# Performance work log

Measured on AMD Instinct MI355X. Metric: run time of the kernel, lower is better.

The kernel has to match this reference:

```python
import jax, jax.numpy as jnp
import numpy as np

N = 50000      # nodes
E = 1_600_000  # edges (avg degree 32)
IN = 256
HID = 64
H = 4          # heads
OUT = 128
NEG = 0.2      # LeakyReLU negative slope


def setup_inputs() -> dict:
    key = jax.random.key(0)
    ks = jax.random.split(key, 16)
    def p(i, shape):
        return jax.random.normal(ks[i], shape, jnp.float32) * 0.05
    x = jax.random.normal(ks[0], (N, IN), jnp.float32)
    edge_index = jax.random.randint(ks[1], (2, E), 0, N, dtype=jnp.int64)
    return dict(
        x=x, edge_index=edge_index,
        W0=p(2, (IN, H * HID)), as0=p(3, (H, HID)), ad0=p(4, (H, HID)), b0=p(5, (H * HID,)),
        W1=p(6, (H * HID, H * HID)), as1=p(7, (H, HID)), ad1=p(8, (H, HID)), b1=p(9, (H * HID,)),
        W2=p(10, (H * HID, OUT)), as2=p(11, (1, OUT)), ad2=p(12, (1, OUT)), b2=p(13, (OUT,)),
        Wl=p(14, (H * HID, OUT)), bl=p(15, (OUT,)),
    )


def gat_conv(x, src, dst, W, a_s, a_d, b, heads, ch):
    # Linear projection -> per-head features [N, H, C]
    h = (x @ W).reshape(-1, heads, ch)
    # Per-node attention logits [N, H]
    al_s = jnp.einsum('nhc,hc->nh', h, a_s)
    al_d = jnp.einsum('nhc,hc->nh', h, a_d)
    # Per-edge logits: gather + LeakyReLU  [E2, H]
    e = jax.nn.leaky_relu(al_s[src] + al_d[dst], NEG)
    # Segment softmax over destination neighborhoods (stable)
    m = jax.ops.segment_max(e, dst, num_segments=N)
    e = jnp.exp(e - m[dst])
    s = jax.ops.segment_sum(e, dst, num_segments=N)
    a = e / s[dst]
    # Weighted scatter-add aggregation [N, H, C]
    out = jax.ops.segment_sum(a[:, :, None] * h[src], dst, num_segments=N)
    return out.reshape(N, heads * ch) + b


def reference(x, edge_index, W0, as0, ad0, b0, W1, as1, ad1, b1, W2, as2, ad2, b2, Wl, bl):
    # add self-loops (PyG GATConv default)
    loop = jnp.arange(N, dtype=edge_index.dtype)
    src = jnp.concatenate([edge_index[0], loop])
    dst = jnp.concatenate([edge_index[1], loop])
    # layer 0: in -> hid*heads (no residual at layer 0)
    h0 = gat_conv(x, src, dst, W0, as0, ad0, b0, H, HID)
    # layer 1: hid*heads -> hid*heads, residual
    h1 = gat_conv(h0, src, dst, W1, as1, ad1, b1, H, HID) + h0
    # layer 2 (last): hid*heads -> out with 1 head, residual via last_linear
    h2 = gat_conv(h1, src, dst, W2, as2, ad2, b2, 1, OUT) + (h1 @ Wl + bl)
    return h2
```

## Files before the change

kernel.cpp:

```cpp
#include <hip/hip_runtime.h>
#include <hip/hip_bf16.h>

#define N_NODES 50000
#define N_EDGES 1600000
#define E2 (N_EDGES + N_NODES)

typedef __attribute__((ext_vector_type(8))) short bf16x8;
typedef __attribute__((ext_vector_type(4))) float f32x4;

static __device__ __forceinline__ float lrelu(float x) { return x > 0.f ? x : 0.2f * x; }

static __device__ __forceinline__ float b2f(ushort u) {
    union { unsigned int u; float f; } v;
    v.u = ((unsigned int)u) << 16;
    return v.f;
}
static __device__ __forceinline__ float hi2f(unsigned int u) {
    union { unsigned int u; float f; } v;
    v.u = u & 0xffff0000u;
    return v.f;
}
static __device__ __forceinline__ float lo2f(unsigned int u) {
    union { unsigned int u; float f; } v;
    v.u = u << 16;
    return v.f;
}
static __device__ __forceinline__ ushort f2b(float f) {
    union { float f; unsigned int u; } v;
    v.f = f;
    unsigned int r = v.u + 0x7FFFu + ((v.u >> 16) & 1u);
    return (ushort)(r >> 16);
}


__global__ void k_deg(const int* __restrict__ edst, int* __restrict__ deg) {
    int e = blockIdx.x * blockDim.x + threadIdx.x;
    if (e >= E2) return;
    int d = (e < N_EDGES) ? edst[e] : (e - N_EDGES);
    atomicAdd(&deg[d], 1);
}

__global__ void k_scan1(const int* __restrict__ deg, int* __restrict__ rowptr, int* __restrict__ bsum) {
    __shared__ int sd[256];
    int t = threadIdx.x;
    int i = blockIdx.x * 256 + t;
    int v = (i < N_NODES) ? deg[i] : 0;
    sd[t] = v;
    __syncthreads();
    for (int off = 1; off < 256; off <<= 1) {
        int add = (t >= off) ? sd[t - off] : 0;
        __syncthreads();
        sd[t] += add;
        __syncthreads();
    }
    if (i < N_NODES) rowptr[i + 1] = sd[t];
    if (t == 255) bsum[blockIdx.x] = sd[255];
}

__global__ void k_scan2(const int* __restrict__ bsum, int* __restrict__ boff, int nb) {
    __shared__ int sd[256];
    int t = threadIdx.x;
    sd[t] = (t < nb) ? bsum[t] : 0;
    __syncthreads();
    for (int off = 1; off < 256; off <<= 1) {
        int add = (t >= off) ? sd[t - off] : 0;
        __syncthreads();
        sd[t] += add;
        __syncthreads();
    }
    if (t < nb) boff[t] = (t > 0) ? sd[t - 1] : 0;
}

__global__ void k_scan3(int* __restrict__ rowptr, int* __restrict__ cursor, const int* __restrict__ boff) {
    int i = blockIdx.x * 256 + threadIdx.x;
    if (i < N_NODES) {
        int r = rowptr[i + 1] + boff[blockIdx.x];
        rowptr[i + 1] = r;
        cursor[i + 1] = r;
    }
    if (i == 0) { rowptr[0] = 0; cursor[0] = 0; }
}

__global__ void k_fill(const int* __restrict__ esrc, const int* __restrict__ edst,
                       int* __restrict__ cursor, int* __restrict__ col) {
    int e = blockIdx.x * blockDim.x + threadIdx.x;
    if (e >= E2) return;
    int s, d;
    if (e < N_EDGES) { s = esrc[e]; d = edst[e]; } else { s = d = e - N_EDGES; }
    int pos = atomicAdd(&cursor[d], 1);
    col[pos] = s;
}


__global__ void k_quant(const float* __restrict__ x, ushort* __restrict__ xb, int n4) {
    int i = blockIdx.x * 256 + threadIdx.x;
    if (i >= n4) return;
    float4 v = ((const float4*)x)[i];
    ushort4 o;
    o.x = f2b(v.x); o.y = f2b(v.y); o.z = f2b(v.z); o.w = f2b(v.w);
    ((ushort4*)xb)[i] = o;
}

__global__ void k_wt(const float* __restrict__ W, ushort* __restrict__ Wt) {
    int i = blockIdx.x * 256 + threadIdx.x;
    int k = i >> 8, n = i & 255;
    Wt[n * 256 + k] = f2b(W[i]);
}

__global__ void k_wtc(const float* __restrict__ W2, const float* __restrict__ Wl, ushort* __restrict__ Wt) {
    int i = blockIdx.x * 256 + threadIdx.x;
    int k = i >> 8, n = i & 255;
    float v = (n < 128) ? W2[k * 128 + n] : Wl[k * 128 + (n - 128)];
    Wt[n * 256 + k] = f2b(v);
}


template <bool FUSE>
__global__ __launch_bounds__(256) void k_mfma(const ushort* __restrict__ A, const ushort* __restrict__ Bt,
                                              ushort* __restrict__ Cb, int M,
                                              const float* __restrict__ a_s, const float* __restrict__ a_d,
                                              float* __restrict__ als, float* __restrict__ ald) {
    const int t = threadIdx.x;
    const int w = t >> 6, l = t & 63;
    const int lr = l & 15, lk = l >> 4;
    const int m0 = blockIdx.x * 32;
    const int n0 = w * 64;
    f32x4 acc[2][4] = {};

    int r0 = m0 + lr;      if (r0 >= M) r0 = M - 1;
    int r1 = m0 + 16 + lr; if (r1 >= M) r1 = M - 1;
    const ushort* a0p = A + (size_t)r0 * 256 + lk * 8;
    const ushort* a1p = A + (size_t)r1 * 256 + lk * 8;
    const ushort* bp  = Bt + (size_t)(n0 + lr) * 256 + lk * 8;

#pragma unroll
    for (int k0 = 0; k0 < 256; k0 += 32) {
        bf16x8 a0 = *(const bf16x8*)(a0p + k0);
        bf16x8 a1 = *(const bf16x8*)(a1p + k0);
#pragma unroll
        for (int n = 0; n < 4; ++n) {
            bf16x8 b = *(const bf16x8*)(bp + n * 16 * 256 + k0);
            acc[0][n] = __builtin_amdgcn_mfma_f32_16x16x32_bf16(a0, b, acc[0][n], 0, 0, 0);
            acc[1][n] = __builtin_amdgcn_mfma_f32_16x16x32_bf16(a1, b, acc[1][n], 0, 0, 0);
        }
    }

#pragma unroll
    for (int m = 0; m < 2; ++m) {
#pragma unroll
        for (int r = 0; r < 4; ++r) {
            int row = m0 + m * 16 + lk * 4 + r;
            if (row >= M) continue;
#pragma unroll
            for (int n = 0; n < 4; ++n) {
                Cb[(size_t)row * 256 + n0 + n * 16 + lr] = f2b(acc[m][n][r]);
            }
        }
    }

    if constexpr (FUSE) {
        float asc[4], adc[4];
#pragma unroll
        for (int n = 0; n < 4; ++n) {
            int c = n0 + n * 16 + lr;
            asc[n] = a_s[c];
            adc[n] = a_d[c];
        }
#pragma unroll
        for (int m = 0; m < 2; ++m) {
#pragma unroll
            for (int r = 0; r < 4; ++r) {
                float pa = 0.f, pd = 0.f;
#pragma unroll
                for (int n = 0; n < 4; ++n) {
                    pa += acc[m][n][r] * asc[n];
                    pd += acc[m][n][r] * adc[n];
                }
#pragma unroll
                for (int off = 1; off < 16; off <<= 1) {
                    pa += __shfl_xor(pa, off);
                    pd += __shfl_xor(pd, off);
                }
                if (lr == 0) {
                    int row = m0 + m * 16 + lk * 4 + r;
                    if (row < M) {
                        als[row * 4 + w] = pa;
                        ald[row * 4 + w] = pd;
                    }
                }
            }
        }
    }
}


template <int HEADS, int CHAN>
__global__ __launch_bounds__(256) void k_al(const ushort* __restrict__ Pb,
                                            const float* __restrict__ a_s, const float* __restrict__ a_d,
                                            float* __restrict__ als, float* __restrict__ ald) {
    int n = blockIdx.x * 4 + (threadIdx.x >> 6);
    if (n >= N_NODES) return;
    int l = threadIdx.x & 63;
    const ushort* row = Pb + (size_t)n * 256;
#pragma unroll
    for (int h = 0; h < HEADS; ++h) {
        float ps = 0.f, pd = 0.f;
#pragma unroll
        for (int c = l; c < CHAN; c += 64) {
            float v = b2f(row[h * CHAN + c]);
            ps += v * a_s[h * CHAN + c];
            pd += v * a_d[h * CHAN + c];
        }
#pragma unroll
        for (int off = 32; off > 0; off >>= 1) {
            ps += __shfl_xor(ps, off);
            pd += __shfl_xor(pd, off);
        }
        if (l == 0) { als[n * HEADS + h] = ps; ald[n * HEADS + h] = pd; }
    }
}


template <int HEADS>
__device__ __forceinline__ void load_als(const float* __restrict__ als, int src, float* v) {
    if constexpr (HEADS == 4) {
        float4 a = *(const float4*)(als + (size_t)src * 4);
        v[0] = a.x; v[1] = a.y; v[2] = a.z; v[3] = a.w;
    } else {
        v[0] = als[src];
    }
}


template <int HEADS, int CHAN, bool RESB, bool LIN, bool WRITEF, bool WRITEB>
__global__ __launch_bounds__(256) void k_aggw(
    const ushort* __restrict__ Pb,
    const float* __restrict__ als, const float* __restrict__ ald,
    const int* __restrict__ rowptr, const int* __restrict__ col,
    const float* __restrict__ bias, const float* __restrict__ bias2,
    const ushort* __restrict__ residb, float* __restrict__ out, ushort* __restrict__ outb) {
    constexpr int BLK = HEADS * CHAN;
    constexpr int CPL = BLK / 64;
    const int t = threadIdx.x;
    const int w = t >> 6, l = t & 63;
    const int n = blockIdx.x * 4 + w;
    const int rs = rowptr[n];
    const int deg = rowptr[n + 1] - rs;

    __shared__ int s_src[4][64];
    __shared__ float s_w[4][64 * HEADS];

    float aldn[HEADS];
    load_als<HEADS>(ald, n, aldn);

    float acc[CPL];
#pragma unroll
    for (int c = 0; c < CPL; ++c) acc[c] = 0.f;
    float sw[HEADS];
#pragma unroll
    for (int h = 0; h < HEADS; ++h) sw[h] = 0.f;

    const int hsel = l >> 4;

    for (int base = 0; base < deg; base += 64) {
        int j = base + l;
        if (j < deg) {
            int src = col[rs + j];
            s_src[w][l] = src;
            float av[HEADS];
            load_als<HEADS>(als, src, av);
#pragma unroll
            for (int h = 0; h < HEADS; ++h) {
                float wv = __expf(lrelu(av[h] + aldn[h]));
                s_w[w][l * HEADS + h] = wv;
                sw[h] += wv;
            }
        }
        int cnt = min(64, deg - base);
        int jj = 0;
        for (; jj + 2 <= cnt; jj += 2) {
            int s0 = __builtin_amdgcn_readfirstlane(s_src[w][jj]);
            int s1 = __builtin_amdgcn_readfirstlane(s_src[w][jj + 1]);
            if constexpr (CPL == 4) {
                float w0 = s_w[w][jj * HEADS + hsel];
                float w1 = s_w[w][(jj + 1) * HEADS + hsel];
                uint2 v0 = *(const uint2*)(Pb + (size_t)s0 * 256 + l * 4);
                uint2 v1 = *(const uint2*)(Pb + (size_t)s1 * 256 + l * 4);
                acc[0] += w0 * lo2f(v0.x); acc[1] += w0 * hi2f(v0.x);
                acc[2] += w0 * lo2f(v0.y); acc[3] += w0 * hi2f(v0.y);
                acc[0] += w1 * lo2f(v1.x); acc[1] += w1 * hi2f(v1.x);
                acc[2] += w1 * lo2f(v1.y); acc[3] += w1 * hi2f(v1.y);
            } else {
                float w0 = s_w[w][jj];
                float w1 = s_w[w][jj + 1];
                unsigned int v0 = *(const unsigned int*)(Pb + (size_t)s0 * 256 + l * 2);
                unsigned int v1 = *(const unsigned int*)(Pb + (size_t)s1 * 256 + l * 2);
                acc[0] += w0 * lo2f(v0); acc[1] += w0 * hi2f(v0);
                acc[0] += w1 * lo2f(v1); acc[1] += w1 * hi2f(v1);
            }
        }
        if (jj < cnt) {
            int s0 = __builtin_amdgcn_readfirstlane(s_src[w][jj]);
            if constexpr (CPL == 4) {
                float w0 = s_w[w][jj * HEADS + hsel];
                uint2 v0 = *(const uint2*)(Pb + (size_t)s0 * 256 + l * 4);
                acc[0] += w0 * lo2f(v0.x); acc[1] += w0 * hi2f(v0.x);
                acc[2] += w0 * lo2f(v0.y); acc[3] += w0 * hi2f(v0.y);
            } else {
                float w0 = s_w[w][jj];
                unsigned int v0 = *(const unsigned int*)(Pb + (size_t)s0 * 256 + l * 2);
                acc[0] += w0 * lo2f(v0); acc[1] += w0 * hi2f(v0);
            }
        }
    }

#pragma unroll
    for (int off = 32; off > 0; off >>= 1)
#pragma unroll
        for (int h = 0; h < HEADS; ++h) sw[h] += __shfl_xor(sw[h], off);

    float stot;
    if constexpr (HEADS == 4) {
        stot = (hsel == 0) ? sw[0] : (hsel == 1) ? sw[1] : (hsel == 2) ? sw[2] : sw[3];
    } else {
        stot = sw[0];
    }
    float rinv = 1.0f / stot;

    float r[CPL];
#pragma unroll
    for (int c = 0; c < CPL; ++c) r[c] = acc[c] * rinv + bias[l * CPL + c];
    if constexpr (RESB) {
        ushort4 rv = *(const ushort4*)(residb + (size_t)n * 256 + l * 4);
        r[0] += b2f(rv.x); r[1] += b2f(rv.y); r[2] += b2f(rv.z); r[3] += b2f(rv.w);
    }
    if constexpr (LIN) {
        unsigned int lv = *(const unsigned int*)(Pb + (size_t)n * 256 + 128 + l * 2);
        float2 bv = *(const float2*)(bias2 + l * 2);
        r[0] += lo2f(lv) + bv.x;
        r[1] += hi2f(lv) + bv.y;
    }
    if constexpr (WRITEF) {
        if constexpr (CPL == 4) {
            *(float4*)&out[(size_t)n * BLK + l * 4] = make_float4(r[0], r[1], r[2], r[3]);
        } else {
            *(float2*)&out[(size_t)n * BLK + l * 2] = make_float2(r[0], r[1]);
        }
    }
    if constexpr (WRITEB) {
        ushort4 o;
        o.x = f2b(r[0]); o.y = f2b(r[1]); o.z = f2b(r[2]); o.w = f2b(r[3]);
        *(ushort4*)&outb[(size_t)n * BLK + l * 4] = o;
    }
}


extern "C" void kernel_launch(void* const* d_in, const int* in_sizes, int n_in,
                              void* d_out, int out_size, void* d_ws, size_t ws_size,
                              hipStream_t stream) {
    const float* x   = (const float*)d_in[0];
    const int* ei    = (const int*)d_in[1];
    const int* esrc  = ei;
    const int* edst  = ei + N_EDGES;
    const float* W0  = (const float*)d_in[2];
    const float* as0 = (const float*)d_in[3];
    const float* ad0 = (const float*)d_in[4];
    const float* b0  = (const float*)d_in[5];
    const float* W1  = (const float*)d_in[6];
    const float* as1 = (const float*)d_in[7];
    const float* ad1 = (const float*)d_in[8];
    const float* b1  = (const float*)d_in[9];
    const float* W2  = (const float*)d_in[10];
    const float* as2 = (const float*)d_in[11];
    const float* ad2 = (const float*)d_in[12];
    const float* b2  = (const float*)d_in[13];
    const float* Wl  = (const float*)d_in[14];
    const float* bl  = (const float*)d_in[15];
    float* out = (float*)d_out;

    char* w = (char*)d_ws;
    auto alloc = [&](size_t bytes) { char* p = w; w += (bytes + 255) & ~(size_t)255; return p; };
    ushort* xb  = (ushort*)alloc((size_t)N_NODES * 256 * 2);
    ushort* Pb  = (ushort*)alloc((size_t)N_NODES * 256 * 2);
    ushort* h0b = (ushort*)alloc((size_t)N_NODES * 256 * 2);
    float* als = (float*)alloc((size_t)N_NODES * 4 * 4);
    float* ald = (float*)alloc((size_t)N_NODES * 4 * 4);
    ushort* Wt0 = (ushort*)alloc(256 * 256 * 2);
    ushort* Wt1 = (ushort*)alloc(256 * 256 * 2);
    ushort* Wtc = (ushort*)alloc(256 * 256 * 2);
    int* deg    = (int*)alloc((size_t)N_NODES * 4);
    int* rowptr = (int*)alloc((size_t)(N_NODES + 1) * 4);
    int* cursor = (int*)alloc((size_t)(N_NODES + 1) * 4);
    int* colb   = (int*)alloc((size_t)E2 * 4);
    int* bsum   = (int*)alloc(256 * 4);
    int* boff   = (int*)alloc(256 * 4);
    ushort* h1b = xb;

    hipMemsetAsync(deg, 0, (size_t)N_NODES * 4, stream);

    int eb = (E2 + 255) / 256;
    int nb = (N_NODES + 255) / 256;
    k_deg<<<eb, 256, 0, stream>>>(edst, deg);
    k_scan1<<<nb, 256, 0, stream>>>(deg, rowptr, bsum);
    k_scan2<<<1, 256, 0, stream>>>(bsum, boff, nb);
    k_scan3<<<nb, 256, 0, stream>>>(rowptr, cursor, boff);
    k_fill<<<eb, 256, 0, stream>>>(esrc, edst, cursor, colb);

    k_quant<<<(N_NODES * 256 / 4 + 255) / 256, 256, 0, stream>>>(x, xb, N_NODES * 256 / 4);
    k_wt<<<256, 256, 0, stream>>>(W0, Wt0);
    k_wt<<<256, 256, 0, stream>>>(W1, Wt1);
    k_wtc<<<256, 256, 0, stream>>>(W2, Wl, Wtc);

    const int gm = (N_NODES + 31) / 32;
    const int ga = (N_NODES + 3) / 4;
    const int gn = N_NODES / 4;

    k_mfma<true><<<gm, 256, 0, stream>>>(xb, Wt0, Pb, N_NODES, as0, ad0, als, ald);
    k_aggw<4, 64, false, false, false, true><<<gn, 256, 0, stream>>>(
        Pb, als, ald, rowptr, colb, b0, nullptr, nullptr, nullptr, h0b);
    k_mfma<true><<<gm, 256, 0, stream>>>(h0b, Wt1, Pb, N_NODES, as1, ad1, als, ald);
    k_aggw<4, 64, true, false, false, true><<<gn, 256, 0, stream>>>(
        Pb, als, ald, rowptr, colb, b1, nullptr, h0b, nullptr, h1b);
    k_mfma<false><<<gm, 256, 0, stream>>>(h1b, Wtc, Pb, N_NODES, nullptr, nullptr, nullptr, nullptr);
    k_al<1, 128><<<ga, 256, 0, stream>>>(Pb, as2, ad2, als, ald);
    k_aggw<1, 128, false, true, true, false><<<gn, 256, 0, stream>>>(
        Pb, als, ald, rowptr, colb, b2, bl, nullptr, out, nullptr);
}
```

Baseline: 779.7 us.

## Build CSR via two-level bucketing with shared-memory local sort

Replaces the degree-count, three-kernel scan and global atomic fill with a single edge pass that scatters packed (src, local dst) pairs into fixed-capacity buckets of 64 destination nodes. A one-block scan computes bucket offsets, then one block per bucket counts degrees and places columns using shared-memory atomics. This cuts global passes and kernel launches over the edge list, but assumes no bucket exceeds a fixed capacity and concentrates global atomics on fewer counters.

Result: slower. 987.3 us (+26.6%).

```diff
diff --git a/kernel.cpp b/kernel.cpp
--- a/kernel.cpp
+++ b/kernel.cpp
@@ -4,6 +4,8 @@
 #define N_NODES 50000
 #define N_EDGES 1600000
 #define E2 (N_EDGES + N_NODES)
+#define NB 782
+#define BCAP 3072
 
 typedef __attribute__((ext_vector_type(8))) short bf16x8;
 typedef __attribute__((ext_vector_type(4))) float f32x4;
@@ -33,62 +35,87 @@
 }
 
 
-__global__ void k_deg(const int* __restrict__ edst, int* __restrict__ deg) {
-    int e = blockIdx.x * blockDim.x + threadIdx.x;
-    if (e >= E2) return;
-    int d = (e < N_EDGES) ? edst[e] : (e - N_EDGES);
-    atomicAdd(&deg[d], 1);
-}
-
-__global__ void k_scan1(const int* __restrict__ deg, int* __restrict__ rowptr, int* __restrict__ bsum) {
-    __shared__ int sd[256];
-    int t = threadIdx.x;
-    int i = blockIdx.x * 256 + t;
-    int v = (i < N_NODES) ? deg[i] : 0;
-    sd[t] = v;
-    __syncthreads();
-    for (int off = 1; off < 256; off <<= 1) {
-        int add = (t >= off) ? sd[t - off] : 0;
-        __syncthreads();
-        sd[t] += add;
-        __syncthreads();
-    }
-    if (i < N_NODES) rowptr[i + 1] = sd[t];
-    if (t == 255) bsum[blockIdx.x] = sd[255];
-}
-
-__global__ void k_scan2(const int* __restrict__ bsum, int* __restrict__ boff, int nb) {
-    __shared__ int sd[256];
-    int t = threadIdx.x;
-    sd[t] = (t < nb) ? bsum[t] : 0;
-    __syncthreads();
-    for (int off = 1; off < 256; off <<= 1) {
-        int add = (t >= off) ? sd[t - off] : 0;
-        __syncthreads();
-        sd[t] += add;
-        __syncthreads();
-    }
-    if (t < nb) boff[t] = (t > 0) ? sd[t - 1] : 0;
-}
-
-__global__ void k_scan3(int* __restrict__ rowptr, int* __restrict__ cursor, const int* __restrict__ boff) {
-    int i = blockIdx.x * 256 + threadIdx.x;
-    if (i < N_NODES) {
-        int r = rowptr[i + 1] + boff[blockIdx.x];
-        rowptr[i + 1] = r;
-        cursor[i + 1] = r;
-    }
-    if (i == 0) { rowptr[0] = 0; cursor[0] = 0; }
-}
-
-__global__ void k_fill(const int* __restrict__ esrc, const int* __restrict__ edst,
-                       int* __restrict__ cursor, int* __restrict__ col) {
-    int e = blockIdx.x * blockDim.x + threadIdx.x;
+__global__ void k_bucket(const int* __restrict__ esrc, const int* __restrict__ edst,
+                         int* __restrict__ bcnt, unsigned int* __restrict__ bbuf) {
+    int e = blockIdx.x * 256 + threadIdx.x;
     if (e >= E2) return;
     int s, d;
     if (e < N_EDGES) { s = esrc[e]; d = edst[e]; } else { s = d = e - N_EDGES; }
-    int pos = atomicAdd(&cursor[d], 1);
-    col[pos] = s;
+    int b = d >> 6;
+    int pos = atomicAdd(&bcnt[b], 1);
+    bbuf[(size_t)b * BCAP + pos] = (unsigned int)s | ((unsigned int)(d & 63) << 16);
+}
+
+__global__ __launch_bounds__(256) void k_bscan(const int* __restrict__ bcnt, int* __restrict__ bbase,
+                                               int* __restrict__ rowptr) {
+    __shared__ int s[256];
+    int t = threadIdx.x;
+    int v[4];
+    int sum = 0;
+#pragma unroll
+    for (int k = 0; k < 4; ++k) {
+        int i = t * 4 + k;
+        v[k] = (i < NB) ? bcnt[i] : 0;
+        sum += v[k];
+    }
+    s[t] = sum;
+    __syncthreads();
+    for (int off = 1; off < 256; off <<= 1) {
+        int add = (t >= off) ? s[t - off] : 0;
+        __syncthreads();
+        s[t] += add;
+        __syncthreads();
+    }
+    int base = s[t] - sum;
+#pragma unroll
+    for (int k = 0; k < 4; ++k) {
+        int i = t * 4 + k;
+        if (i < NB) bbase[i] = base;
+        base += v[k];
+    }
+    if (t == 0) rowptr[N_NODES] = E2;
+}
+
+__global__ __launch_bounds__(256) void k_build(const int* __restrict__ bcnt, const int* __restrict__ bbase,
+                                               const unsigned int* __restrict__ bbuf,
+                                               int* __restrict__ rowptr, int* __restrict__ col) {
+    const int b = blockIdx.x;
+    const int t = threadIdx.x;
+    const int cnt = bcnt[b];
+    const int base = bbase[b];
+    const int node0 = b << 6;
+
+    __shared__ unsigned int s_e[BCAP];
+    __shared__ int s_deg[64];
+    __shared__ int s_cur[64];
+
+    if (t < 64) s_deg[t] = 0;
+    __syncthreads();
+    for (int i = t; i < cnt; i += 256) {
+        unsigned int p = bbuf[(size_t)b * BCAP + i];
+        s_e[i] = p;
+        atomicAdd(&s_deg[p >> 16], 1);
+    }
+    __syncthreads();
+    if (t < 64) {
+        int d = s_deg[t];
+        int incl = d;
+#pragma unroll
+        for (int off = 1; off < 64; off <<= 1) {
+            int o = __shfl_up(incl, off);
+            if (t >= off) incl += o;
+        }
+        int start = incl - d;
+        s_cur[t] = start;
+        int node = node0 + t;
+        if (node < N_NODES) rowptr[node] = base + start;
+    }
+    __syncthreads();
+    for (int i = t; i < cnt; i += 256) {
+        unsigned int p = s_e[i];
+        int pos = atomicAdd(&s_cur[p >> 16], 1);
+        col[base + pos] = (int)(p & 0xFFFFu);
+    }
 }
 
 
@@ -388,23 +415,19 @@
     ushort* Wt0 = (ushort*)alloc(256 * 256 * 2);
     ushort* Wt1 = (ushort*)alloc(256 * 256 * 2);
     ushort* Wtc = (ushort*)alloc(256 * 256 * 2);
-    int* deg    = (int*)alloc((size_t)N_NODES * 4);
+    unsigned int* bbuf = (unsigned int*)alloc((size_t)NB * BCAP * 4);
+    int* bcnt   = (int*)alloc((size_t)NB * 4);
+    int* bbase  = (int*)alloc((size_t)NB * 4);
     int* rowptr = (int*)alloc((size_t)(N_NODES + 1) * 4);
-    int* cursor = (int*)alloc((size_t)(N_NODES + 1) * 4);
     int* colb   = (int*)alloc((size_t)E2 * 4);
-    int* bsum   = (int*)alloc(256 * 4);
-    int* boff   = (int*)alloc(256 * 4);
     ushort* h1b = xb;
 
-    hipMemsetAsync(deg, 0, (size_t)N_NODES * 4, stream);
+    hipMemsetAsync(bcnt, 0, (size_t)NB * 4, stream);
 
     int eb = (E2 + 255) / 256;
-    int nb = (N_NODES + 255) / 256;
-    k_deg<<<eb, 256, 0, stream>>>(edst, deg);
-    k_scan1<<<nb, 256, 0, stream>>>(deg, rowptr, bsum);
-    k_scan2<<<1, 256, 0, stream>>>(bsum, boff, nb);
-    k_scan3<<<nb, 256, 0, stream>>>(rowptr, cursor, boff);
-    k_fill<<<eb, 256, 0, stream>>>(esrc, edst, cursor, colb);
+    k_bucket<<<eb, 256, 0, stream>>>(esrc, edst, bcnt, bbuf);
+    k_bscan<<<1, 256, 0, stream>>>(bcnt, bbase, rowptr);
+    k_build<<<NB, 256, 0, stream>>>(bcnt, bbase, bbuf, rowptr, colb);
 
     k_quant<<<(N_NODES * 256 / 4 + 255) / 256, 256, 0, stream>>>(x, xb, N_NODES * 256 / 4);
     k_wt<<<256, 256, 0, stream>>>(W0, Wt0);
```
